# Kernel tuning notes

Hardware: AMD Instinct MI355X
Metric: run time of the kernel (lower is better)

The kernel has to match this reference:

```python
import jax, jax.numpy as jnp
import numpy as np

EPS = 1e-5

def setup_inputs() -> dict:
    key = jax.random.key(0)
    B, N, F_in, F_out = 8, 2048, 64, 64
    ks = jax.random.split(key, 8)
    batch_nb_nodes = jax.random.randint(ks[0], (B,), N // 2, N + 1).astype(jnp.int32)
    node_mask = (jnp.arange(N)[None, :] < batch_nb_nodes[:, None]).astype(jnp.float32)  # [B,N]
    adj_mask = node_mask[:, :, None] * node_mask[:, None, :]                            # [B,N,N]
    emb_in = jax.random.normal(ks[1], (B, N, F_in), jnp.float32) * node_mask[:, :, None]
    adj_in = jax.random.uniform(ks[2], (B, N, N), jnp.float32) * adj_mask
    kernel_sigma = jnp.asarray(float(F_in), jnp.float32)          # gaussian kernel bandwidth
    combine_w = jnp.array([0.5, 0.5], jnp.float32)                # affine combine of [adj_in, kernel]
    conv_W = jax.random.normal(ks[3], (2 * F_in, F_out), jnp.float32) / np.float32(np.sqrt(2 * F_in))
    conv_b = jnp.zeros((F_out,), jnp.float32)
    nu_W = jax.random.normal(ks[4], (F_in + F_out, F_out), jnp.float32) / np.float32(np.sqrt(F_in + F_out))
    nu_b = jnp.zeros((F_out,), jnp.float32)
    return {"emb_in": emb_in, "adj_in": adj_in, "adj_mask": adj_mask,
            "batch_nb_nodes": batch_nb_nodes, "kernel_sigma": kernel_sigma,
            "combine_w": combine_w, "conv_W": conv_W, "conv_b": conv_b,
            "nu_W": nu_W, "nu_b": nu_b}

def reference(emb_in, adj_in, adj_mask, batch_nb_nodes, kernel_sigma, combine_w, conv_W, conv_b, nu_W, nu_b):
    B, N, F = emb_in.shape
    # --- gaussian kernel adjacency update: K_ij = exp(-||e_i - e_j||^2 / sigma) ---
    sq = jnp.sum(emb_in * emb_in, axis=-1)                                  # [B,N]
    d2 = sq[:, :, None] + sq[:, None, :] - 2.0 * jnp.einsum('bif,bjf->bij', emb_in, emb_in)
    ker = jnp.exp(-jnp.maximum(d2, 0.0) / kernel_sigma)                     # [B,N,N]
    # --- affine combine of previous adjacency and kernel matrices, then mask ---
    adj = (combine_w[0] * adj_in + combine_w[1] * ker) * adj_mask           # [B,N,N]
    # --- spatialnorm: per-graph mean/std over valid nodes (layer_nb != 0) ---
    node_mask = (jnp.arange(N)[None, :] < batch_nb_nodes[:, None]).astype(emb_in.dtype)  # [B,N]
    cnt = jnp.maximum(batch_nb_nodes.astype(emb_in.dtype), 1.0)[:, None, None]
    m = node_mask[:, :, None]
    mean = jnp.sum(emb_in * m, axis=1, keepdims=True) / cnt                 # [B,1,F]
    var = jnp.sum(((emb_in - mean) ** 2) * m, axis=1, keepdims=True) / cnt  # [B,1,F]
    emb_n = ((emb_in - mean) / jnp.sqrt(var + EPS)) * m                     # mask_embedding
    # --- operators: degree (D @ x) and adjacency (A @ x), joined then conv ---
    deg = jnp.sum(adj, axis=-1)                                             # [B,N]
    op_deg = deg[:, :, None] * emb_n                                        # [B,N,F]
    op_adj = jnp.einsum('bij,bjf->bif', adj, emb_n)                         # [B,N,F]
    emb_upd = jnp.concatenate([op_deg, op_adj], axis=-1) @ conv_W + conv_b  # [B,N,F_out]
    # --- node update: relu(W [emb_in ; emb_update] + b) ---
    emb = jax.nn.relu(jnp.concatenate([emb_in, emb_upd], axis=-1) @ nu_W + nu_b)
    return emb, adj
```

## Files before the change

### kernel.cpp

```cpp
#include <hip/hip_runtime.h>
#include <math.h>

#define BB 8
#define NN 2048
#define FF 64
#define EPSV 1e-5f
#define EMB_SZ (BB * NN * FF)

#define WS_SQ    0
#define WS_ASUM  (BB * NN)
#define WS_ASQ   (WS_ASUM + BB * FF)
#define WS_MEAN  (WS_ASQ + BB * FF)
#define WS_RSTD  (WS_MEAN + BB * FF)
#define WS_DEG   (WS_RSTD + BB * FF)

typedef __attribute__((ext_vector_type(8))) short bf16x8;
typedef __attribute__((ext_vector_type(4))) float f32x4;

__device__ inline unsigned short f2bf(float x) {
    union { float f; unsigned u; } v; v.f = x;
    return (unsigned short)((v.u + 0x7fffu + ((v.u >> 16) & 1u)) >> 16);
}
__device__ inline float bf2f(unsigned short h) {
    union { float f; unsigned u; } v; v.u = ((unsigned)h) << 16;
    return v.f;
}

__global__ __launch_bounds__(256) void k_stats(const float* __restrict__ emb,
                                               float* __restrict__ sq,
                                               float* __restrict__ asum,
                                               float* __restrict__ asq) {
    const int b    = blockIdx.y;
    const int lane = threadIdx.x & 63;
    const int grp  = threadIdx.x >> 6;
    const int base_i = blockIdx.x << 6;

    float s = 0.f, q = 0.f;
    for (int it = 0; it < 16; ++it) {
        const int i = base_i + (it << 2) + grp;
        const float x = emb[((size_t)(b * NN + i) << 6) + lane];
        const float x2 = x * x;
        s += x;
        q += x2;
        float r = x2;
        r += __shfl_xor(r, 1);
        r += __shfl_xor(r, 2);
        r += __shfl_xor(r, 4);
        r += __shfl_xor(r, 8);
        r += __shfl_xor(r, 16);
        r += __shfl_xor(r, 32);
        if (lane == 0) sq[b * NN + i] = r;
    }
    __shared__ float redS[4][64];
    __shared__ float redQ[4][64];
    redS[grp][lane] = s;
    redQ[grp][lane] = q;
    __syncthreads();
    if (threadIdx.x < 64) {
        const float ts = redS[0][lane] + redS[1][lane] + redS[2][lane] + redS[3][lane];
        const float tq = redQ[0][lane] + redQ[1][lane] + redQ[2][lane] + redQ[3][lane];
        atomicAdd(&asum[(b << 6) + lane], ts);
        atomicAdd(&asq[(b << 6) + lane], tq);
    }
}

__global__ void k_finalize(const float* __restrict__ asum, const float* __restrict__ asq,
                           const int* __restrict__ nbp,
                           float* __restrict__ mean, float* __restrict__ rstd) {
    const int t = threadIdx.x;
    const int b = t >> 6;
    const float cnt = fmaxf((float)nbp[b], 1.f);
    const float m = asum[t] / cnt;
    float v = asq[t] / cnt - m * m;
    v = fmaxf(v, 0.f);
    mean[t] = m;
    rstd[t] = rsqrtf(v + EPSV);
}

__global__ __launch_bounds__(256, 4) void k_adj_deg(const float* __restrict__ emb,
                                                    const float* __restrict__ adj_in,
                                                    const float* __restrict__ sq,
                                                    const float* __restrict__ sigp,
                                                    const float* __restrict__ cw,
                                                    const int* __restrict__ nbp,
                                                    float* __restrict__ adj_out,
                                                    float* __restrict__ deg) {
    __shared__ __align__(16) unsigned short Ah[64][40];
    __shared__ __align__(16) unsigned short Al[64][40];
    __shared__ __align__(16) unsigned short Bh[128][40];
    __shared__ __align__(16) unsigned short Bl[128][40];

    const int b  = blockIdx.z;
    const int j0 = blockIdx.x << 7;
    const int i0 = blockIdx.y << 6;
    const int nb = nbp[b];
    const int bN = b * NN;
    const int tid = threadIdx.x;

    if (i0 >= nb || j0 >= nb) {
        const float4 z = make_float4(0.f, 0.f, 0.f, 0.f);
#pragma unroll
        for (int qq = 0; qq < 8; ++qq) {
            const int idx = tid * 8 + qq;
            const int row = idx >> 5, c4 = (idx & 31) << 2;
            *(float4*)(adj_out + ((size_t)(bN + i0 + row) << 11) + j0 + c4) = z;
        }
        return;
    }

    const int w   = tid >> 6;
    const int lane = tid & 63;
    const int l15 = lane & 15, lq = lane >> 4;

    f32x4 acc[8];
#pragma unroll
    for (int c = 0; c < 8; ++c) acc[c] = (f32x4){0.f, 0.f, 0.f, 0.f};

    for (int kh = 0; kh < 64; kh += 32) {
        {
            const int row = tid >> 1, kc = (tid & 1) << 4;
            const float* src = emb + ((size_t)(bN + j0 + row) << 6) + kh + kc;
            __align__(16) float xv[16];
            *(float4*)(xv + 0)  = *(const float4*)(src + 0);
            *(float4*)(xv + 4)  = *(const float4*)(src + 4);
            *(float4*)(xv + 8)  = *(const float4*)(src + 8);
            *(float4*)(xv + 12) = *(const float4*)(src + 12);
            __align__(16) unsigned short hh[16], ll[16];
#pragma unroll
            for (int e = 0; e < 16; ++e) {
                hh[e] = f2bf(xv[e]);
                ll[e] = f2bf(xv[e] - bf2f(hh[e]));
            }
            *(bf16x8*)&Bh[row][kc]     = *(bf16x8*)&hh[0];
            *(bf16x8*)&Bh[row][kc + 8] = *(bf16x8*)&hh[8];
            *(bf16x8*)&Bl[row][kc]     = *(bf16x8*)&ll[0];
            *(bf16x8*)&Bl[row][kc + 8] = *(bf16x8*)&ll[8];
        }
        if (tid < 128) {
            const int row = tid >> 1, kc = (tid & 1) << 4;
            const float* src = emb + ((size_t)(bN + i0 + row) << 6) + kh + kc;
            __align__(16) float xv[16];
            *(float4*)(xv + 0)  = *(const float4*)(src + 0);
            *(float4*)(xv + 4)  = *(const float4*)(src + 4);
            *(float4*)(xv + 8)  = *(const float4*)(src + 8);
            *(float4*)(xv + 12) = *(const float4*)(src + 12);
            __align__(16) unsigned short hh[16], ll[16];
#pragma unroll
            for (int e = 0; e < 16; ++e) {
                hh[e] = f2bf(xv[e]);
                ll[e] = f2bf(xv[e] - bf2f(hh[e]));
            }
            *(bf16x8*)&Ah[row][kc]     = *(bf16x8*)&hh[0];
            *(bf16x8*)&Ah[row][kc + 8] = *(bf16x8*)&hh[8];
            *(bf16x8*)&Al[row][kc]     = *(bf16x8*)&ll[0];
            *(bf16x8*)&Al[row][kc + 8] = *(bf16x8*)&ll[8];
        }
        __syncthreads();

        const bf16x8 ah = *(bf16x8*)&Ah[w * 16 + l15][lq * 8];
        const bf16x8 al = *(bf16x8*)&Al[w * 16 + l15][lq * 8];
#pragma unroll
        for (int c = 0; c < 8; ++c) {
            const bf16x8 bh = *(bf16x8*)&Bh[c * 16 + l15][lq * 8];
            const bf16x8 bl = *(bf16x8*)&Bl[c * 16 + l15][lq * 8];
            acc[c] = __builtin_amdgcn_mfma_f32_16x16x32_bf16(ah, bh, acc[c], 0, 0, 0);
            acc[c] = __builtin_amdgcn_mfma_f32_16x16x32_bf16(ah, bl, acc[c], 0, 0, 0);
            acc[c] = __builtin_amdgcn_mfma_f32_16x16x32_bf16(al, bh, acc[c], 0, 0, 0);
        }
        __syncthreads();
    }

    const float inv_sigma = 1.0f / sigp[0];
    const float w0 = cw[0], w1 = cw[1];

    float sqi[4], sqj[8];
    const int irow0 = i0 + w * 16 + lq * 4;
#pragma unroll
    for (int r = 0; r < 4; ++r) sqi[r] = sq[bN + irow0 + r];
#pragma unroll
    for (int c = 0; c < 8; ++c) sqj[c] = sq[bN + j0 + c * 16 + l15];

#pragma unroll
    for (int r = 0; r < 4; ++r) {
        const int gi = irow0 + r;
        const float mi = (gi < nb) ? 1.f : 0.f;
        float ain[8];
#pragma unroll
        for (int c = 0; c < 8; ++c)
            ain[c] = adj_in[((size_t)(bN + gi) << 11) + j0 + c * 16 + l15];
        float rsum = 0.f;
#pragma unroll
        for (int c = 0; c < 8; ++c) {
            const int gj = j0 + c * 16 + l15;
            float d2 = sqi[r] + sqj[c] - 2.f * acc[c][r];
            d2 = fmaxf(d2, 0.f);
            const float ker = __expf(-d2 * inv_sigma);
            const float mv = (gj < nb) ? mi : 0.f;
            const float o = (w0 * ain[c] + w1 * ker) * mv;
            adj_out[((size_t)(bN + gi) << 11) + gj] = o;
            rsum += o;
        }
        rsum += __shfl_xor(rsum, 1);
        rsum += __shfl_xor(rsum, 2);
        rsum += __shfl_xor(rsum, 4);
        rsum += __shfl_xor(rsum, 8);
        if (l15 == 0) atomicAdd(&deg[bN + gi], rsum);
    }
}

__global__ __launch_bounds__(256, 4) void k_opadj(const float* __restrict__ adj,
                                                  const float* __restrict__ emb,
                                                  const float* __restrict__ meanp,
                                                  const float* __restrict__ rstdp,
                                                  const int* __restrict__ nbp,
                                                  float* __restrict__ opadj) {
    __shared__ __align__(16) unsigned short As[64][72];
    __shared__ __align__(16) unsigned short Bt[64][72];

    const int b  = blockIdx.z;
    const int i0 = blockIdx.x << 6;
    const int nb = nbp[b];
    if (i0 >= nb) return;
    const int jbeg = blockIdx.y << 9;
    if (jbeg >= nb) return;
    const int jend = min(jbeg + 512, (nb + 63) & ~63);

    const int bN = b * NN;
    const int tid = threadIdx.x;
    const int w = tid >> 6, lane = tid & 63;
    const int l15 = lane & 15, lq = lane >> 4;

    const int sjj = tid & 63;
    const int fb  = (tid >> 6) << 4;
    float mn[16], rs[16];
#pragma unroll
    for (int e = 0; e < 16; e += 4) {
        *(float4*)&mn[e] = *(const float4*)(meanp + (b << 6) + fb + e);
        *(float4*)&rs[e] = *(const float4*)(rstdp + (b << 6) + fb + e);
    }

    f32x4 acc[4];
#pragma unroll
    for (int c = 0; c < 4; ++c) acc[c] = (f32x4){0.f, 0.f, 0.f, 0.f};

    for (int jt = jbeg; jt < jend; jt += 64) {
        {
            const int row = tid >> 2, jc = (tid & 3) << 4;
            const float* src = adj + ((size_t)(bN + i0 + row) << 11) + jt + jc;
            __align__(16) float xv[16];
            *(float4*)(xv + 0)  = *(const float4*)(src + 0);
            *(float4*)(xv + 4)  = *(const float4*)(src + 4);
            *(float4*)(xv + 8)  = *(const float4*)(src + 8);
            *(float4*)(xv + 12) = *(const float4*)(src + 12);
            __align__(16) unsigned short hh[16];
#pragma unroll
            for (int e = 0; e < 16; ++e) hh[e] = f2bf(xv[e]);
            *(bf16x8*)&As[row][jc]     = *(bf16x8*)&hh[0];
            *(bf16x8*)&As[row][jc + 8] = *(bf16x8*)&hh[8];
        }
        {
            const float msk = (jt + sjj < nb) ? 1.f : 0.f;
            const float* src = emb + ((size_t)(bN + jt + sjj) << 6) + fb;
            __align__(16) float xv[16];
            *(float4*)(xv + 0)  = *(const float4*)(src + 0);
            *(float4*)(xv + 4)  = *(const float4*)(src + 4);
            *(float4*)(xv + 8)  = *(const float4*)(src + 8);
            *(float4*)(xv + 12) = *(const float4*)(src + 12);
#pragma unroll
            for (int e = 0; e < 16; ++e) {
                const float en = (xv[e] - mn[e]) * rs[e] * msk;
                Bt[fb + e][sjj] = f2bf(en);
            }
        }
        __syncthreads();
#pragma unroll
        for (int ks = 0; ks < 2; ++ks) {
            const bf16x8 a = *(bf16x8*)&As[w * 16 + l15][ks * 32 + lq * 8];
#pragma unroll
            for (int c = 0; c < 4; ++c) {
                const bf16x8 bv = *(bf16x8*)&Bt[c * 16 + l15][ks * 32 + lq * 8];
                acc[c] = __builtin_amdgcn_mfma_f32_16x16x32_bf16(a, bv, acc[c], 0, 0, 0);
            }
        }
        __syncthreads();
    }

#pragma unroll
    for (int c = 0; c < 4; ++c)
#pragma unroll
        for (int r = 0; r < 4; ++r) {
            const int gi = i0 + w * 16 + lq * 4 + r;
            atomicAdd(opadj + ((size_t)(bN + gi) << 6) + c * 16 + l15, acc[c][r]);
        }
}

__global__ __launch_bounds__(256) void k_epilogue(const float* __restrict__ emb,
                                                  const float* __restrict__ meanp,
                                                  const float* __restrict__ rstdp,
                                                  const float* __restrict__ degp,
                                                  const int* __restrict__ nbp,
                                                  const float* __restrict__ convW,
                                                  const float* __restrict__ convB,
                                                  const float* __restrict__ nuW,
                                                  const float* __restrict__ nuB,
                                                  float* __restrict__ emb_out) {
    __shared__ __align__(16) float smem[13056];
    float* xs = smem;
    float* us = smem + 8704;
    float* es = smem;

    const int b   = blockIdx.y;
    const int i0  = blockIdx.x << 6;
    const int tid = threadIdx.x;
    const int tx = tid & 15, ty = tid >> 4;
    const int nb = nbp[b];
    const int bN = b * NN;
    const int sj  = tid >> 2;
    const int scb = (tid & 3) << 4;

    {
        const float4 m4 = *(const float4*)(meanp + (b << 6) + (tx << 2));
        const float4 r4 = *(const float4*)(rstdp + (b << 6) + (tx << 2));
#pragma unroll
        for (int u = 0; u < 4; ++u) {
            const int il = (ty << 2) + u;
            const int gi = i0 + il;
            const float msk = (gi < nb) ? 1.f : 0.f;
            const float dg = degp[bN + gi];
            const float4 v = *(const float4*)(emb + ((size_t)(bN + gi) << 6) + (tx << 2));
            float4 en;
            en.x = (v.x - m4.x) * r4.x * msk;
            en.y = (v.y - m4.y) * r4.y * msk;
            en.z = (v.z - m4.z) * r4.z * msk;
            en.w = (v.w - m4.w) * r4.w * msk;
            float4 od;
            od.x = dg * en.x; od.y = dg * en.y; od.z = dg * en.z; od.w = dg * en.w;
            *(float4*)&xs[il * 132 + (tx << 2)] = od;
            const float4 oa = *(const float4*)(emb_out + ((size_t)(bN + gi) << 6) + (tx << 2));
            *(float4*)&xs[il * 132 + 64 + (tx << 2)] = oa;
        }
    }
    __syncthreads();

    {
        float u4[4][4];
#pragma unroll
        for (int r = 0; r < 4; ++r)
#pragma unroll
            for (int c = 0; c < 4; ++c) u4[r][c] = 0.f;
        for (int fis = 0; fis < 128; fis += 4) {
            const float4 w0v = *(const float4*)(convW + ((fis + 0) << 6) + (tx << 2));
            const float4 w1v = *(const float4*)(convW + ((fis + 1) << 6) + (tx << 2));
            const float4 w2v = *(const float4*)(convW + ((fis + 2) << 6) + (tx << 2));
            const float4 w3v = *(const float4*)(convW + ((fis + 3) << 6) + (tx << 2));
#pragma unroll
            for (int r = 0; r < 4; ++r) {
                const float4 x = *(const float4*)&xs[((ty << 2) + r) * 132 + fis];
                u4[r][0] += x.x * w0v.x + x.y * w1v.x + x.z * w2v.x + x.w * w3v.x;
                u4[r][1] += x.x * w0v.y + x.y * w1v.y + x.z * w2v.y + x.w * w3v.y;
                u4[r][2] += x.x * w0v.z + x.y * w1v.z + x.z * w2v.z + x.w * w3v.z;
                u4[r][3] += x.x * w0v.w + x.y * w1v.w + x.z * w2v.w + x.w * w3v.w;
            }
        }
        const float4 cb4 = *(const float4*)(convB + (tx << 2));
#pragma unroll
        for (int r = 0; r < 4; ++r) {
            float4 o;
            o.x = u4[r][0] + cb4.x; o.y = u4[r][1] + cb4.y;
            o.z = u4[r][2] + cb4.z; o.w = u4[r][3] + cb4.w;
            *(float4*)&us[((ty << 2) + r) * 68 + (tx << 2)] = o;
        }
    }
    __syncthreads();

    {
        const float* pe = emb + ((size_t)(bN + i0 + sj) << 6) + scb;
#pragma unroll
        for (int u = 0; u < 4; ++u)
            *(float4*)&es[sj * 68 + scb + (u << 2)] = *(const float4*)(pe + (u << 2));
    }
    __syncthreads();

    {
        float u4[4][4];
#pragma unroll
        for (int r = 0; r < 4; ++r)
#pragma unroll
            for (int c = 0; c < 4; ++c) u4[r][c] = 0.f;
        for (int fis = 0; fis < 64; fis += 4) {
            const float4 w0v = *(const float4*)(nuW + ((fis + 0) << 6) + (tx << 2));
            const float4 w1v = *(const float4*)(nuW + ((fis + 1) << 6) + (tx << 2));
            const float4 w2v = *(const float4*)(nuW + ((fis + 2) << 6) + (tx << 2));
            const float4 w3v = *(const float4*)(nuW + ((fis + 3) << 6) + (tx << 2));
#pragma unroll
            for (int r = 0; r < 4; ++r) {
                const float4 x = *(const float4*)&es[((ty << 2) + r) * 68 + fis];
                u4[r][0] += x.x * w0v.x + x.y * w1v.x + x.z * w2v.x + x.w * w3v.x;
                u4[r][1] += x.x * w0v.y + x.y * w1v.y + x.z * w2v.y + x.w * w3v.y;
                u4[r][2] += x.x * w0v.z + x.y * w1v.z + x.z * w2v.z + x.w * w3v.z;
                u4[r][3] += x.x * w0v.w + x.y * w1v.w + x.z * w2v.w + x.w * w3v.w;
            }
        }
        for (int fis = 0; fis < 64; fis += 4) {
            const float4 w0v = *(const float4*)(nuW + ((64 + fis + 0) << 6) + (tx << 2));
            const float4 w1v = *(const float4*)(nuW + ((64 + fis + 1) << 6) + (tx << 2));
            const float4 w2v = *(const float4*)(nuW + ((64 + fis + 2) << 6) + (tx << 2));
            const float4 w3v = *(const float4*)(nuW + ((64 + fis + 3) << 6) + (tx << 2));
#pragma unroll
            for (int r = 0; r < 4; ++r) {
                const float4 x = *(const float4*)&us[((ty << 2) + r) * 68 + fis];
                u4[r][0] += x.x * w0v.x + x.y * w1v.x + x.z * w2v.x + x.w * w3v.x;
                u4[r][1] += x.x * w0v.y + x.y * w1v.y + x.z * w2v.y + x.w * w3v.y;
                u4[r][2] += x.x * w0v.z + x.y * w1v.z + x.z * w2v.z + x.w * w3v.z;
                u4[r][3] += x.x * w0v.w + x.y * w1v.w + x.z * w2v.w + x.w * w3v.w;
            }
        }
        const float4 nb4 = *(const float4*)(nuB + (tx << 2));
#pragma unroll
        for (int r = 0; r < 4; ++r) {
            const int gi = i0 + (ty << 2) + r;
            float4 o;
            o.x = fmaxf(u4[r][0] + nb4.x, 0.f);
            o.y = fmaxf(u4[r][1] + nb4.y, 0.f);
            o.z = fmaxf(u4[r][2] + nb4.z, 0.f);
            o.w = fmaxf(u4[r][3] + nb4.w, 0.f);
            *(float4*)(emb_out + ((size_t)(bN + gi) << 6) + (tx << 2)) = o;
        }
    }
}

extern "C" void kernel_launch(void* const* d_in, const int* in_sizes, int n_in,
                              void* d_out, int out_size, void* d_ws, size_t ws_size,
                              hipStream_t stream) {
    (void)in_sizes; (void)n_in; (void)out_size; (void)ws_size;
    const float* emb_in   = (const float*)d_in[0];
    const float* adj_in   = (const float*)d_in[1];
    const int*   nbp      = (const int*)d_in[3];
    const float* sigp     = (const float*)d_in[4];
    const float* cw       = (const float*)d_in[5];
    const float* convW    = (const float*)d_in[6];
    const float* convB    = (const float*)d_in[7];
    const float* nuW      = (const float*)d_in[8];
    const float* nuB      = (const float*)d_in[9];

    float* emb_out = (float*)d_out;
    float* adj_out = (float*)d_out + EMB_SZ;

    float* ws   = (float*)d_ws;
    float* sq   = ws + WS_SQ;
    float* asum = ws + WS_ASUM;
    float* asq  = ws + WS_ASQ;
    float* mean = ws + WS_MEAN;
    float* rstd = ws + WS_RSTD;
    float* deg  = ws + WS_DEG;

    hipMemsetAsync(asum, 0, (2 * BB * FF + 2 * BB * FF + BB * NN) * sizeof(float) / 2
                            + (BB * NN) * sizeof(float) / 1, stream);
    hipMemsetAsync(emb_out, 0, (size_t)EMB_SZ * sizeof(float), stream);

    k_stats<<<dim3(32, BB), 256, 0, stream>>>(emb_in, sq, asum, asq);
    k_finalize<<<1, BB * FF, 0, stream>>>(asum, asq, nbp, mean, rstd);
    k_adj_deg<<<dim3(NN / 128, NN / 64, BB), 256, 0, stream>>>(emb_in, adj_in, sq, sigp,
                                                               cw, nbp, adj_out, deg);
    k_opadj<<<dim3(NN / 64, 4, BB), 256, 0, stream>>>(adj_out, emb_in, mean, rstd,
                                                      nbp, emb_out);
    k_epilogue<<<dim3(NN / 64, BB), 256, 0, stream>>>(emb_in, mean, rstd, deg, nbp,
                                                      convW, convB, nuW, nuB, emb_out);
}
```

Measured before the change: 395.2 us.

## Fuse adjacency build with A@x GEMM and precompute bf16 embeddings

Merges the kernel-adjacency/degree kernel and the adjacency-times-normalized-embedding kernel into one. The computed adjacency tile is converted to bf16 in shared memory and multiplied straight away, so adj_out is no longer read back from global memory. A new prep kernel precomputes the bf16 embeddings and a transposed normalized copy. The Gram product also drops the hi/lo split-bf16 trick and uses single bf16, which costs precision in the distance term. Shared-memory tiles use XOR swizzling to avoid bank conflicts.

```diff
diff --git a/kernel.cpp b/kernel.cpp
--- a/kernel.cpp
+++ b/kernel.cpp
@@ -7,23 +7,21 @@
 #define EPSV 1e-5f
 #define EMB_SZ (BB * NN * FF)
 
-#define WS_SQ    0
-#define WS_ASUM  (BB * NN)
-#define WS_ASQ   (WS_ASUM + BB * FF)
-#define WS_MEAN  (WS_ASQ + BB * FF)
-#define WS_RSTD  (WS_MEAN + BB * FF)
-#define WS_DEG   (WS_RSTD + BB * FF)
+#define WS_SQ      0
+#define WS_ASUM    (BB * NN)
+#define WS_ASQ     (WS_ASUM + BB * FF)
+#define WS_MEAN    (WS_ASQ + BB * FF)
+#define WS_RSTD    (WS_MEAN + BB * FF)
+#define WS_DEG     (WS_RSTD + BB * FF)
+#define WS_F32_END (WS_DEG + BB * NN)
 
 typedef __attribute__((ext_vector_type(8))) short bf16x8;
 typedef __attribute__((ext_vector_type(4))) float f32x4;
-
-__device__ inline unsigned short f2bf(float x) {
+typedef unsigned short ushort_t;
+
+__device__ inline ushort_t f2bf(float x) {
     union { float f; unsigned u; } v; v.f = x;
-    return (unsigned short)((v.u + 0x7fffu + ((v.u >> 16) & 1u)) >> 16);
-}
-__device__ inline float bf2f(unsigned short h) {
-    union { float f; unsigned u; } v; v.u = ((unsigned)h) << 16;
-    return v.f;
+    return (ushort_t)((v.u + 0x7fffu + ((v.u >> 16) & 1u)) >> 16);
 }
 
 __global__ __launch_bounds__(256) void k_stats(const float* __restrict__ emb,
@@ -77,221 +75,198 @@
     rstd[t] = rsqrtf(v + EPSV);
 }
 
-__global__ __launch_bounds__(256, 4) void k_adj_deg(const float* __restrict__ emb,
-                                                    const float* __restrict__ adj_in,
-                                                    const float* __restrict__ sq,
-                                                    const float* __restrict__ sigp,
-                                                    const float* __restrict__ cw,
-                                                    const int* __restrict__ nbp,
-                                                    float* __restrict__ adj_out,
-                                                    float* __restrict__ deg) {
-    __shared__ __align__(16) unsigned short Ah[64][40];
-    __shared__ __align__(16) unsigned short Al[64][40];
-    __shared__ __align__(16) unsigned short Bh[128][40];
-    __shared__ __align__(16) unsigned short Bl[128][40];
-
-    const int b  = blockIdx.z;
-    const int j0 = blockIdx.x << 7;
-    const int i0 = blockIdx.y << 6;
-    const int nb = nbp[b];
-    const int bN = b * NN;
-    const int tid = threadIdx.x;
-
-    if (i0 >= nb || j0 >= nb) {
-        const float4 z = make_float4(0.f, 0.f, 0.f, 0.f);
-#pragma unroll
-        for (int qq = 0; qq < 8; ++qq) {
-            const int idx = tid * 8 + qq;
-            const int row = idx >> 5, c4 = (idx & 31) << 2;
-            *(float4*)(adj_out + ((size_t)(bN + i0 + row) << 11) + j0 + c4) = z;
-        }
-        return;
-    }
-
-    const int w   = tid >> 6;
-    const int lane = tid & 63;
+__global__ __launch_bounds__(256) void k_prep(const float* __restrict__ emb,
+                                              const float* __restrict__ meanp,
+                                              const float* __restrict__ rstdp,
+                                              const int* __restrict__ nbp,
+                                              ushort_t* __restrict__ embBf,
+                                              ushort_t* __restrict__ embnT) {
+    __shared__ __align__(16) ushort_t T[64][72];
+    const int b = blockIdx.y, j0 = blockIdx.x << 6;
+    const int nb = nbp[b], bN = b * NN;
+    const int t = threadIdx.x;
+    const int j = t >> 2, fs = (t & 3) << 4;
+
+    float mn[16], rs[16];
+#pragma unroll
+    for (int e = 0; e < 16; e += 4) {
+        *(float4*)&mn[e] = *(const float4*)(meanp + (b << 6) + fs + e);
+        *(float4*)&rs[e] = *(const float4*)(rstdp + (b << 6) + fs + e);
+    }
+    const float msk = (j0 + j < nb) ? 1.f : 0.f;
+    const float* src = emb + ((size_t)(bN + j0 + j) << 6) + fs;
+    __align__(16) float x[16];
+    *(float4*)(x + 0)  = *(const float4*)(src + 0);
+    *(float4*)(x + 4)  = *(const float4*)(src + 4);
+    *(float4*)(x + 8)  = *(const float4*)(src + 8);
+    *(float4*)(x + 12) = *(const float4*)(src + 12);
+    __align__(16) ushort_t raw[16];
+#pragma unroll
+    for (int e = 0; e < 16; ++e) {
+        raw[e] = f2bf(x[e]);
+        T[fs + e][j] = f2bf((x[e] - mn[e]) * rs[e] * msk);
+    }
+    ushort_t* dst = embBf + ((size_t)(bN + j0 + j) << 6) + fs;
+    *(bf16x8*)dst       = *(bf16x8*)&raw[0];
+    *(bf16x8*)(dst + 8) = *(bf16x8*)&raw[8];
+    __syncthreads();
+    const int f = t >> 2, js = (t & 3) << 4;
+    const bf16x8 v0 = *(bf16x8*)&T[f][js];
+    const bf16x8 v1 = *(bf16x8*)&T[f][js + 8];
+    ushort_t* dstT = embnT + ((size_t)(b * FF + f) << 11) + j0 + js;
+    *(bf16x8*)dstT       = v0;
+    *(bf16x8*)(dstT + 8) = v1;
+}
+
+__global__ __launch_bounds__(256, 4) void k_adj(const ushort_t* __restrict__ embBf,
+                                                const ushort_t* __restrict__ embnT,
+                                                const float* __restrict__ adj_in,
+                                                const float* __restrict__ sq,
+                                                const float* __restrict__ sigp,
+                                                const float* __restrict__ cw,
+                                                const int* __restrict__ nbp,
+                                                float* __restrict__ adj_out,
+                                                float* __restrict__ deg,
+                                                float* __restrict__ opadj) {
+    __shared__ __align__(16) ushort_t BgA[8192];
+    __shared__ __align__(16) ushort_t EnT[8192];
+
+    const int b = blockIdx.z, i0 = blockIdx.y << 6, jbeg = blockIdx.x << 9;
+    const int nb = nbp[b], bN = b * NN;
+    const int tid = threadIdx.x, w = tid >> 6, lane = tid & 63;
     const int l15 = lane & 15, lq = lane >> 4;
-
-    f32x4 acc[8];
-#pragma unroll
-    for (int c = 0; c < 8; ++c) acc[c] = (f32x4){0.f, 0.f, 0.f, 0.f};
-
-    for (int kh = 0; kh < 64; kh += 32) {
-        {
-            const int row = tid >> 1, kc = (tid & 1) << 4;
-            const float* src = emb + ((size_t)(bN + j0 + row) << 6) + kh + kc;
-            __align__(16) float xv[16];
-            *(float4*)(xv + 0)  = *(const float4*)(src + 0);
-            *(float4*)(xv + 4)  = *(const float4*)(src + 4);
-            *(float4*)(xv + 8)  = *(const float4*)(src + 8);
-            *(float4*)(xv + 12) = *(const float4*)(src + 12);
-            __align__(16) unsigned short hh[16], ll[16];
-#pragma unroll
-            for (int e = 0; e < 16; ++e) {
-                hh[e] = f2bf(xv[e]);
-                ll[e] = f2bf(xv[e] - bf2f(hh[e]));
-            }
-            *(bf16x8*)&Bh[row][kc]     = *(bf16x8*)&hh[0];
-            *(bf16x8*)&Bh[row][kc + 8] = *(bf16x8*)&hh[8];
-            *(bf16x8*)&Bl[row][kc]     = *(bf16x8*)&ll[0];
-            *(bf16x8*)&Bl[row][kc + 8] = *(bf16x8*)&ll[8];
-        }
-        if (tid < 128) {
-            const int row = tid >> 1, kc = (tid & 1) << 4;
-            const float* src = emb + ((size_t)(bN + i0 + row) << 6) + kh + kc;
-            __align__(16) float xv[16];
-            *(float4*)(xv + 0)  = *(const float4*)(src + 0);
-            *(float4*)(xv + 4)  = *(const float4*)(src + 4);
-            *(float4*)(xv + 8)  = *(const float4*)(src + 8);
-            *(float4*)(xv + 12) = *(const float4*)(src + 12);
-            __align__(16) unsigned short hh[16], ll[16];
-#pragma unroll
-            for (int e = 0; e < 16; ++e) {
-                hh[e] = f2bf(xv[e]);
-                ll[e] = f2bf(xv[e] - bf2f(hh[e]));
-            }
-            *(bf16x8*)&Ah[row][kc]     = *(bf16x8*)&hh[0];
-            *(bf16x8*)&Ah[row][kc + 8] = *(bf16x8*)&hh[8];
-            *(bf16x8*)&Al[row][kc]     = *(bf16x8*)&ll[0];
-            *(bf16x8*)&Al[row][kc + 8] = *(bf16x8*)&ll[8];
-        }
-        __syncthreads();
-
-        const bf16x8 ah = *(bf16x8*)&Ah[w * 16 + l15][lq * 8];
-        const bf16x8 al = *(bf16x8*)&Al[w * 16 + l15][lq * 8];
-#pragma unroll
-        for (int c = 0; c < 8; ++c) {
-            const bf16x8 bh = *(bf16x8*)&Bh[c * 16 + l15][lq * 8];
-            const bf16x8 bl = *(bf16x8*)&Bl[c * 16 + l15][lq * 8];
-            acc[c] = __builtin_amdgcn_mfma_f32_16x16x32_bf16(ah, bh, acc[c], 0, 0, 0);
-            acc[c] = __builtin_amdgcn_mfma_f32_16x16x32_bf16(ah, bl, acc[c], 0, 0, 0);
-            acc[c] = __builtin_amdgcn_mfma_f32_16x16x32_bf16(al, bh, acc[c], 0, 0, 0);
-        }
-        __syncthreads();
-    }
+    const int xk = (l15 & 7) << 4;
+    const bool rowlive = (i0 < nb);
+    const int nbr = (nb + 127) & ~127;
+    const int jend = min(jbeg + 512, nbr);
 
     const float inv_sigma = 1.0f / sigp[0];
     const float w0 = cw[0], w1 = cw[1];
 
-    float sqi[4], sqj[8];
-    const int irow0 = i0 + w * 16 + lq * 4;
-#pragma unroll
-    for (int r = 0; r < 4; ++r) sqi[r] = sq[bN + irow0 + r];
-#pragma unroll
-    for (int c = 0; c < 8; ++c) sqj[c] = sq[bN + j0 + c * 16 + l15];
-
-#pragma unroll
-    for (int r = 0; r < 4; ++r) {
-        const int gi = irow0 + r;
-        const float mi = (gi < nb) ? 1.f : 0.f;
-        float ain[8];
-#pragma unroll
-        for (int c = 0; c < 8; ++c)
-            ain[c] = adj_in[((size_t)(bN + gi) << 11) + j0 + c * 16 + l15];
-        float rsum = 0.f;
-#pragma unroll
-        for (int c = 0; c < 8; ++c) {
-            const int gj = j0 + c * 16 + l15;
-            float d2 = sqi[r] + sqj[c] - 2.f * acc[c][r];
-            d2 = fmaxf(d2, 0.f);
-            const float ker = __expf(-d2 * inv_sigma);
-            const float mv = (gj < nb) ? mi : 0.f;
-            const float o = (w0 * ain[c] + w1 * ker) * mv;
-            adj_out[((size_t)(bN + gi) << 11) + gj] = o;
-            rsum += o;
-        }
-        rsum += __shfl_xor(rsum, 1);
-        rsum += __shfl_xor(rsum, 2);
-        rsum += __shfl_xor(rsum, 4);
-        rsum += __shfl_xor(rsum, 8);
-        if (l15 == 0) atomicAdd(&deg[bN + gi], rsum);
-    }
-}
-
-__global__ __launch_bounds__(256, 4) void k_opadj(const float* __restrict__ adj,
-                                                  const float* __restrict__ emb,
-                                                  const float* __restrict__ meanp,
-                                                  const float* __restrict__ rstdp,
-                                                  const int* __restrict__ nbp,
-                                                  float* __restrict__ opadj) {
-    __shared__ __align__(16) unsigned short As[64][72];
-    __shared__ __align__(16) unsigned short Bt[64][72];
-
-    const int b  = blockIdx.z;
-    const int i0 = blockIdx.x << 6;
-    const int nb = nbp[b];
-    if (i0 >= nb) return;
-    const int jbeg = blockIdx.y << 9;
-    if (jbeg >= nb) return;
-    const int jend = min(jbeg + 512, (nb + 63) & ~63);
-
-    const int bN = b * NN;
-    const int tid = threadIdx.x;
-    const int w = tid >> 6, lane = tid & 63;
-    const int l15 = lane & 15, lq = lane >> 4;
-
-    const int sjj = tid & 63;
-    const int fb  = (tid >> 6) << 4;
-    float mn[16], rs[16];
-#pragma unroll
-    for (int e = 0; e < 16; e += 4) {
-        *(float4*)&mn[e] = *(const float4*)(meanp + (b << 6) + fb + e);
-        *(float4*)&rs[e] = *(const float4*)(rstdp + (b << 6) + fb + e);
-    }
-
-    f32x4 acc[4];
-#pragma unroll
-    for (int c = 0; c < 4; ++c) acc[c] = (f32x4){0.f, 0.f, 0.f, 0.f};
-
-    for (int jt = jbeg; jt < jend; jt += 64) {
-        {
-            const int row = tid >> 2, jc = (tid & 3) << 4;
-            const float* src = adj + ((size_t)(bN + i0 + row) << 11) + jt + jc;
-            __align__(16) float xv[16];
-            *(float4*)(xv + 0)  = *(const float4*)(src + 0);
-            *(float4*)(xv + 4)  = *(const float4*)(src + 4);
-            *(float4*)(xv + 8)  = *(const float4*)(src + 8);
-            *(float4*)(xv + 12) = *(const float4*)(src + 12);
-            __align__(16) unsigned short hh[16];
-#pragma unroll
-            for (int e = 0; e < 16; ++e) hh[e] = f2bf(xv[e]);
-            *(bf16x8*)&As[row][jc]     = *(bf16x8*)&hh[0];
-            *(bf16x8*)&As[row][jc + 8] = *(bf16x8*)&hh[8];
-        }
-        {
-            const float msk = (jt + sjj < nb) ? 1.f : 0.f;
-            const float* src = emb + ((size_t)(bN + jt + sjj) << 6) + fb;
-            __align__(16) float xv[16];
-            *(float4*)(xv + 0)  = *(const float4*)(src + 0);
-            *(float4*)(xv + 4)  = *(const float4*)(src + 4);
-            *(float4*)(xv + 8)  = *(const float4*)(src + 8);
-            *(float4*)(xv + 12) = *(const float4*)(src + 12);
-#pragma unroll
-            for (int e = 0; e < 16; ++e) {
-                const float en = (xv[e] - mn[e]) * rs[e] * msk;
-                Bt[fb + e][sjj] = f2bf(en);
-            }
-        }
-        __syncthreads();
-#pragma unroll
-        for (int ks = 0; ks < 2; ++ks) {
-            const bf16x8 a = *(bf16x8*)&As[w * 16 + l15][ks * 32 + lq * 8];
-#pragma unroll
-            for (int c = 0; c < 4; ++c) {
-                const bf16x8 bv = *(bf16x8*)&Bt[c * 16 + l15][ks * 32 + lq * 8];
-                acc[c] = __builtin_amdgcn_mfma_f32_16x16x32_bf16(a, bv, acc[c], 0, 0, 0);
-            }
-        }
-        __syncthreads();
-    }
-
-#pragma unroll
-    for (int c = 0; c < 4; ++c)
+    const int ib = i0 + w * 16;
+    bf16x8 ah0 = {}, ah1 = {};
+    float sqi[4] = {0.f, 0.f, 0.f, 0.f};
+    f32x4 accP[4];
+#pragma unroll
+    for (int c = 0; c < 4; ++c) accP[c] = (f32x4){0.f, 0.f, 0.f, 0.f};
+    float rsum[4] = {0.f, 0.f, 0.f, 0.f};
+
+    if (rowlive) {
+        const ushort_t* ap = embBf + ((size_t)(bN + ib + l15) << 6) + lq * 8;
+        ah0 = *(const bf16x8*)ap;
+        ah1 = *(const bf16x8*)(ap + 32);
+#pragma unroll
+        for (int r = 0; r < 4; ++r) sqi[r] = sq[bN + ib + lq * 4 + r];
+    }
+
+    for (int jt = jbeg; jt < jbeg + 512; jt += 128) {
+        if (rowlive && jt < jend) {
+            {
+                const int row = tid >> 1, fs2 = (tid & 1) << 5;
+                const ushort_t* src = embBf + ((size_t)(bN + jt + row) << 6) + fs2;
+                const int kx = (row & 7) << 4;
+#pragma unroll
+                for (int e = 0; e < 4; ++e) {
+                    const bf16x8 v = *(const bf16x8*)(src + e * 8);
+                    *(bf16x8*)((char*)BgA + (((row << 7) + ((fs2 + e * 8) << 1)) ^ kx)) = v;
+                }
+            }
+            {
+                const int f = tid >> 2, js = (tid & 3) << 5;
+                const ushort_t* src = embnT + ((size_t)(b * FF + f) << 11) + jt + js;
+                const int kx = (f & 7) << 4;
+#pragma unroll
+                for (int e = 0; e < 4; ++e) {
+                    const bf16x8 v = *(const bf16x8*)(src + e * 8);
+                    *(bf16x8*)((char*)EnT + (((f << 8) + ((js + e * 8) << 1)) ^ kx)) = v;
+                }
+            }
+            __syncthreads();
+            f32x4 acc[8];
+#pragma unroll
+            for (int c = 0; c < 8; ++c) acc[c] = (f32x4){0.f, 0.f, 0.f, 0.f};
+#pragma unroll
+            for (int c = 0; c < 8; ++c) {
+                const int lin = ((c * 16 + l15) << 7) + lq * 16;
+                const bf16x8 b0 = *(const bf16x8*)((char*)BgA + (lin ^ xk));
+                const bf16x8 b1 = *(const bf16x8*)((char*)BgA + ((lin + 64) ^ xk));
+                acc[c] = __builtin_amdgcn_mfma_f32_16x16x32_bf16(ah0, b0, acc[c], 0, 0, 0);
+                acc[c] = __builtin_amdgcn_mfma_f32_16x16x32_bf16(ah1, b1, acc[c], 0, 0, 0);
+            }
+            float sqj[8];
+#pragma unroll
+            for (int c = 0; c < 8; ++c) sqj[c] = sq[bN + jt + c * 16 + l15];
+#pragma unroll
+            for (int r = 0; r < 4; ++r) {
+                const int gi = ib + lq * 4 + r;
+                const float mi = (gi < nb) ? 1.f : 0.f;
+                const float* arow = adj_in + ((size_t)(bN + gi) << 11) + jt + l15;
+                float* orow = adj_out + ((size_t)(bN + gi) << 11) + jt + l15;
+#pragma unroll
+                for (int c = 0; c < 8; ++c) {
+                    const int gj = jt + c * 16 + l15;
+                    float d2 = sqi[r] + sqj[c] - 2.f * acc[c][r];
+                    d2 = fmaxf(d2, 0.f);
+                    const float ker = __expf(-d2 * inv_sigma);
+                    const float mv = (gj < nb) ? mi : 0.f;
+                    const float o = (w0 * arow[c * 16] + w1 * ker) * mv;
+                    orow[c * 16] = o;
+                    acc[c][r] = o;
+                    rsum[r] += o;
+                }
+            }
+            __syncthreads();
+#pragma unroll
+            for (int r = 0; r < 4; ++r) {
+                const int iloc = w * 16 + lq * 4 + r;
+                const int kx2 = (iloc & 7) << 4;
+#pragma unroll
+                for (int c = 0; c < 8; ++c) {
+                    const int lin = (iloc << 8) + ((c * 16 + l15) << 1);
+                    *(ushort_t*)((char*)BgA + (lin ^ kx2)) = f2bf(acc[c][r]);
+                }
+            }
+            __syncthreads();
+#pragma unroll
+            for (int ks = 0; ks < 4; ++ks) {
+                const int lina = ((w * 16 + l15) << 8) + ks * 64 + lq * 16;
+                const bf16x8 a = *(const bf16x8*)((char*)BgA + (lina ^ xk));
+#pragma unroll
+                for (int c = 0; c < 4; ++c) {
+                    const int linb = ((c * 16 + l15) << 8) + ks * 64 + lq * 16;
+                    const bf16x8 bv = *(const bf16x8*)((char*)EnT + (linb ^ xk));
+                    accP[c] = __builtin_amdgcn_mfma_f32_16x16x32_bf16(a, bv, accP[c], 0, 0, 0);
+                }
+            }
+            __syncthreads();
+        } else {
+            const float4 z = make_float4(0.f, 0.f, 0.f, 0.f);
+#pragma unroll
+            for (int q = 0; q < 8; ++q) {
+                const int idx = tid * 8 + q;
+                const int row = idx >> 5, c4 = (idx & 31) << 2;
+                *(float4*)(adj_out + ((size_t)(bN + i0 + row) << 11) + jt + c4) = z;
+            }
+        }
+    }
+
+    if (rowlive) {
+        const int irow = ib + lq * 4;
 #pragma unroll
         for (int r = 0; r < 4; ++r) {
-            const int gi = i0 + w * 16 + lq * 4 + r;
-            atomicAdd(opadj + ((size_t)(bN + gi) << 6) + c * 16 + l15, acc[c][r]);
-        }
+            float v = rsum[r];
+            v += __shfl_xor(v, 1);
+            v += __shfl_xor(v, 2);
+            v += __shfl_xor(v, 4);
+            v += __shfl_xor(v, 8);
+            if (l15 == 0) atomicAdd(&deg[bN + irow + r], v);
+        }
+#pragma unroll
+        for (int c = 0; c < 4; ++c)
+#pragma unroll
+            for (int r = 0; r < 4; ++r)
+                atomicAdd(opadj + ((size_t)(bN + irow + r) << 6) + c * 16 + l15, accP[c][r]);
+    }
 }
 
 __global__ __launch_bounds__(256) void k_epilogue(const float* __restrict__ emb,
@@ -453,17 +428,17 @@
     float* mean = ws + WS_MEAN;
     float* rstd = ws + WS_RSTD;
     float* deg  = ws + WS_DEG;
-
-    hipMemsetAsync(asum, 0, (2 * BB * FF + 2 * BB * FF + BB * NN) * sizeof(float) / 2
-                            + (BB * NN) * sizeof(float) / 1, stream);
+    ushort_t* embBf = (ushort_t*)(ws + WS_F32_END);
+    ushort_t* embnT = embBf + (size_t)BB * NN * FF;
+
+    hipMemsetAsync(asum, 0, (WS_F32_END - WS_ASUM) * sizeof(float), stream);
     hipMemsetAsync(emb_out, 0, (size_t)EMB_SZ * sizeof(float), stream);
 
     k_stats<<<dim3(32, BB), 256, 0, stream>>>(emb_in, sq, asum, asq);
     k_finalize<<<1, BB * FF, 0, stream>>>(asum, asq, nbp, mean, rstd);
-    k_adj_deg<<<dim3(NN / 128, NN / 64, BB), 256, 0, stream>>>(emb_in, adj_in, sq, sigp,
-                                                               cw, nbp, adj_out, deg);
-    k_opadj<<<dim3(NN / 64, 4, BB), 256, 0, stream>>>(adj_out, emb_in, mean, rstd,
-                                                      nbp, emb_out);
-    k_epilogue<<<dim3(NN / 64, BB), 256, 0, stream>>>(emb_in, mean, rstd, deg, nbp,
-                                                      convW, convB, nuW, nuB, emb_out);
-}
+    k_prep<<<dim3(32, BB), 256, 0, stream>>>(emb_in, mean, rstd, nbp, embBf, embnT);
+    k_adj<<<dim3(4, 32, BB), 256, 0, stream>>>(embBf, embnT, adj_in, sq, sigp, cw,
+                                               nbp, adj_out, deg, emb_out);
+    k_epilogue<<<dim3(32, BB), 256, 0, stream>>>(emb_in, mean, rstd, deg, nbp,
+                                                 convW, convB, nuW, nuB, emb_out);
+}
```

New measurement: 430.3 us. +8.9%, slower.
